# Kernel optimization log

Hardware: AMD Instinct MI355X
Metric: run time of the kernel (lower is better)

Reference implementation:

```python
import jax, jax.numpy as jnp
import numpy as np

INPUT_SIZE = 24
HIDDEN = 128
N_LAYERS = 2
OUT_SIZE = 1


def setup_inputs() -> dict:
    key = jax.random.key(0)
    ks = jax.random.split(key, 2 + 4 * N_LAYERS + 2)
    x = jax.random.normal(ks[0], (2048, 128, INPUT_SIZE), dtype=jnp.float32)
    params = {}
    s = 1.0 / np.sqrt(HIDDEN)
    idx = 1
    for l in range(N_LAYERS):
        in_dim = INPUT_SIZE if l == 0 else HIDDEN
        params[f"W_ih{l}"] = jax.random.uniform(ks[idx], (4 * HIDDEN, in_dim), minval=-s, maxval=s, dtype=jnp.float32); idx += 1
        params[f"W_hh{l}"] = jax.random.uniform(ks[idx], (4 * HIDDEN, HIDDEN), minval=-s, maxval=s, dtype=jnp.float32); idx += 1
        params[f"b_ih{l}"] = jax.random.uniform(ks[idx], (4 * HIDDEN,), minval=-s, maxval=s, dtype=jnp.float32); idx += 1
        params[f"b_hh{l}"] = jax.random.uniform(ks[idx], (4 * HIDDEN,), minval=-s, maxval=s, dtype=jnp.float32); idx += 1
    params["W_fc"] = jax.random.uniform(ks[idx], (OUT_SIZE, HIDDEN), minval=-s, maxval=s, dtype=jnp.float32); idx += 1
    params["b_fc"] = jax.random.uniform(ks[idx], (OUT_SIZE,), minval=-s, maxval=s, dtype=jnp.float32)
    return {"x": x, **params}


def _lstm_layer(x, W_ih, W_hh, b_ih, b_hh):
    # x: [B, T, in] -> outputs [B, T, H]. PyTorch gate order: i, f, g, o.
    B = x.shape[0]
    H = W_hh.shape[1]
    # precompute input projections for all timesteps: [T, B, 4H]
    xproj = jnp.einsum('bti,gi->tbg', x, W_ih) + b_ih + b_hh

    def step(carry, xp_t):
        h, c = carry
        gates = xp_t + h @ W_hh.T  # [B, 4H]
        i, f, g, o = jnp.split(gates, 4, axis=-1)
        i = jax.nn.sigmoid(i)
        f = jax.nn.sigmoid(f)
        g = jnp.tanh(g)
        o = jax.nn.sigmoid(o)
        c = f * c + i * g
        h = o * jnp.tanh(c)
        return (h, c), h

    h0 = jnp.zeros((B, H), dtype=x.dtype)
    c0 = jnp.zeros((B, H), dtype=x.dtype)
    (_, _), hs = jax.lax.scan(step, (h0, c0), xproj)
    return jnp.transpose(hs, (1, 0, 2))  # [B, T, H]


def reference(x, W_ih0, W_hh0, b_ih0, b_hh0, W_ih1, W_hh1, b_ih1, b_hh1, W_fc, b_fc):
    # Inference-mode forward: inter-layer dropout (p=0.2) is identity in eval.
    h1 = _lstm_layer(x, W_ih0, W_hh0, b_ih0, b_hh0)   # [B, T, H]
    h2 = _lstm_layer(h1, W_ih1, W_hh1, b_ih1, b_hh1)  # [B, T, H]
    last = h2[:, -1, :]                               # [B, H]
    return last @ W_fc.T + b_fc                       # [B, 1]
```

## Files before the change

kernel.cpp:

```cpp
#include <hip/hip_runtime.h>

#define TSTEPS 128
#define NIN 24
#define HD 128
#define BT 16
#define NBLK 128
#define NTH 512

#define RS    136
#define SLOT  (BT*RS)
#define H1B   (2*SLOT)
#define W1B   (4*SLOT)
#define SM_ELTS (W1B + 8*16*512)
#define SM_BYTES (SM_ELTS*2)

typedef _Float16 half8  __attribute__((ext_vector_type(8)));
typedef _Float16 half4v __attribute__((ext_vector_type(4)));
typedef float    floatx4 __attribute__((ext_vector_type(4)));

__device__ __forceinline__ float sigf(float x) {
    return __builtin_amdgcn_rcpf(1.0f + __expf(-x));
}
__device__ __forceinline__ float tanh_f(float x) {
    return 1.0f - 2.0f * __builtin_amdgcn_rcpf(1.0f + __expf(2.0f * x));
}

__device__ __forceinline__ half8 ldw8(const float* p) {
    const float4* q = (const float4*)p;
    float4 a = q[0], b = q[1];
    half8 r;
    r[0] = (_Float16)a.x; r[1] = (_Float16)a.y; r[2] = (_Float16)a.z; r[3] = (_Float16)a.w;
    r[4] = (_Float16)b.x; r[5] = (_Float16)b.y; r[6] = (_Float16)b.z; r[7] = (_Float16)b.w;
    return r;
}

__global__ __launch_bounds__(NTH, 2)
void lstm2_fused(const float* __restrict__ x,
                 const float* __restrict__ Wih0, const float* __restrict__ Whh0,
                 const float* __restrict__ bih0, const float* __restrict__ bhh0,
                 const float* __restrict__ Wih1, const float* __restrict__ Whh1,
                 const float* __restrict__ bih1, const float* __restrict__ bhh1,
                 const float* __restrict__ Wfc,  const float* __restrict__ bfc,
                 float* __restrict__ out)
{
    extern __shared__ __align__(16) _Float16 SM[];

    const int tid = threadIdx.x;
    const int blk = blockIdx.x;
    const int wv  = tid >> 6;
    const int ln  = tid & 63;
    const int qd  = ln >> 4;
    const int nn  = ln & 15;
    const int b0  = blk * BT;
    const int jc  = wv * 16 + nn;

    const half8 z8 = {0, 0, 0, 0, 0, 0, 0, 0};

    for (int i = tid * 8; i < W1B; i += NTH * 8) *(half8*)&SM[i] = z8;

    float bias0[4], bias1[4];
    half8 wih0[4];
    half8 whh0[4][4];
    half8 wih1[4][4];
#pragma unroll
    for (int tI = 0; tI < 4; ++tI) {
        int g = tI * HD + wv * 16 + nn;
        bias0[tI] = bih0[g] + bhh0[g];
        bias1[tI] = bih1[g] + bhh1[g];
        wih0[tI] = (qd < 3) ? ldw8(Wih0 + g * NIN + qd * 8) : z8;
#pragma unroll
        for (int kk = 0; kk < 4; ++kk) {
            whh0[tI][kk] = ldw8(Whh0 + g * HD + kk * 32 + qd * 8);
            wih1[tI][kk] = ldw8(Wih1 + g * HD + kk * 32 + qd * 8);
        }
    }

    for (int i = tid; i < 512 * 32; i += NTH) {
        int g  = i >> 5;
        int k0 = (i & 31) << 2;
        float4 v = *(const float4*)(Whh1 + g * HD + k0);
        half4v h; h[0] = (_Float16)v.x; h[1] = (_Float16)v.y;
                  h[2] = (_Float16)v.z; h[3] = (_Float16)v.w;
        int dst = W1B + ((((g >> 4) & 7) * 16) + (g >> 7) * 4 + (k0 >> 5)) * 512
                      + (((k0 >> 3) & 3) * 16 + (g & 15)) * 8 + (k0 & 7);
        *(half4v*)&SM[dst] = h;
    }

    const float* xrow = x + (size_t)(b0 + nn) * (TSTEPS * NIN) + (qd < 3 ? qd * 8 : 16);
    float4 pf0 = *(const float4*)(xrow);
    float4 pf1 = *(const float4*)(xrow + 4);

    float cs0[4] = {0.f, 0.f, 0.f, 0.f};
    float cs1[4] = {0.f, 0.f, 0.f, 0.f};
    const int w1base = W1B + wv * 8192 + ln * 8;

    __syncthreads();

    {
        half8 ax;
        ax[0] = (_Float16)pf0.x; ax[1] = (_Float16)pf0.y; ax[2] = (_Float16)pf0.z; ax[3] = (_Float16)pf0.w;
        ax[4] = (_Float16)pf1.x; ax[5] = (_Float16)pf1.y; ax[6] = (_Float16)pf1.z; ax[7] = (_Float16)pf1.w;
        pf0 = *(const float4*)(xrow + NIN);
        pf1 = *(const float4*)(xrow + NIN + 4);

        floatx4 acc0[4];
#pragma unroll
        for (int tI = 0; tI < 4; ++tI) {
            floatx4 a0 = {bias0[tI], bias0[tI], bias0[tI], bias0[tI]};
            acc0[tI] = __builtin_amdgcn_mfma_f32_16x16x32_f16(ax, wih0[tI], a0, 0, 0, 0);
        }
#pragma unroll
        for (int r = 0; r < 4; ++r) {
            float iv = sigf(acc0[0][r]);
            float gv = tanh_f(acc0[2][r]);
            float ov = sigf(acc0[3][r]);
            float cn = iv * gv;
            cs0[r] = cn;
            SM[(qd * 4 + r) * RS + jc] = (_Float16)(ov * tanh_f(cn));
        }
    }

#pragma unroll 1
    for (int t = 1; t < TSTEPS; ++t) {
        __syncthreads();

        half8 ax;
        ax[0] = (_Float16)pf0.x; ax[1] = (_Float16)pf0.y; ax[2] = (_Float16)pf0.z; ax[3] = (_Float16)pf0.w;
        ax[4] = (_Float16)pf1.x; ax[5] = (_Float16)pf1.y; ax[6] = (_Float16)pf1.z; ax[7] = (_Float16)pf1.w;
        {
            const int tn = (t < TSTEPS - 1) ? t + 1 : TSTEPS - 1;
            pf0 = *(const float4*)(xrow + tn * NIN);
            pf1 = *(const float4*)(xrow + tn * NIN + 4);
        }

        const int h0r = ((t - 1) & 1) * SLOT;
        const int h0w = (t & 1) * SLOT;
        const int h1r = H1B + (t & 1) * SLOT;
        const int h1w = H1B + ((t & 1) ^ 1) * SLOT;

        floatx4 acc0[4], acc1[4];
#pragma unroll
        for (int tI = 0; tI < 4; ++tI) {
            floatx4 a0 = {bias0[tI], bias0[tI], bias0[tI], bias0[tI]};
            acc0[tI] = __builtin_amdgcn_mfma_f32_16x16x32_f16(ax, wih0[tI], a0, 0, 0, 0);
            floatx4 a1 = {bias1[tI], bias1[tI], bias1[tI], bias1[tI]};
            acc1[tI] = a1;
        }

#pragma unroll
        for (int kk = 0; kk < 4; ++kk) {
            const half8 ah = *(const half8*)&SM[h0r + nn * RS + kk * 32 + qd * 8];
#pragma unroll
            for (int tI = 0; tI < 4; ++tI)
                acc0[tI] = __builtin_amdgcn_mfma_f32_16x16x32_f16(ah, whh0[tI][kk], acc0[tI], 0, 0, 0);
#pragma unroll
            for (int tI = 0; tI < 4; ++tI)
                acc1[tI] = __builtin_amdgcn_mfma_f32_16x16x32_f16(ah, wih1[tI][kk], acc1[tI], 0, 0, 0);
        }

#pragma unroll
        for (int kk = 0; kk < 4; ++kk) {
            const half8 a2 = *(const half8*)&SM[h1r + nn * RS + kk * 32 + qd * 8];
#pragma unroll
            for (int tI = 0; tI < 4; ++tI) {
                const half8 w1 = *(const half8*)&SM[w1base + (tI * 4 + kk) * 512];
                acc1[tI] = __builtin_amdgcn_mfma_f32_16x16x32_f16(a2, w1, acc1[tI], 0, 0, 0);
            }
        }

#pragma unroll
        for (int r = 0; r < 4; ++r) {
            float iv = sigf(acc0[0][r]);
            float fv = sigf(acc0[1][r]);
            float gv = tanh_f(acc0[2][r]);
            float ov = sigf(acc0[3][r]);
            float cn = fv * cs0[r] + iv * gv;
            cs0[r] = cn;
            SM[h0w + (qd * 4 + r) * RS + jc] = (_Float16)(ov * tanh_f(cn));
        }
#pragma unroll
        for (int r = 0; r < 4; ++r) {
            float iv = sigf(acc1[0][r]);
            float fv = sigf(acc1[1][r]);
            float gv = tanh_f(acc1[2][r]);
            float ov = sigf(acc1[3][r]);
            float cn = fv * cs1[r] + iv * gv;
            cs1[r] = cn;
            SM[h1w + (qd * 4 + r) * RS + jc] = (_Float16)(ov * tanh_f(cn));
        }
    }

    {
        __syncthreads();
        floatx4 acc1[4];
#pragma unroll
        for (int tI = 0; tI < 4; ++tI) {
            floatx4 a1 = {bias1[tI], bias1[tI], bias1[tI], bias1[tI]};
            acc1[tI] = a1;
        }
#pragma unroll
        for (int kk = 0; kk < 4; ++kk) {
            const half8 ah = *(const half8*)&SM[SLOT + nn * RS + kk * 32 + qd * 8];
#pragma unroll
            for (int tI = 0; tI < 4; ++tI)
                acc1[tI] = __builtin_amdgcn_mfma_f32_16x16x32_f16(ah, wih1[tI][kk], acc1[tI], 0, 0, 0);
        }
#pragma unroll
        for (int kk = 0; kk < 4; ++kk) {
            const half8 a2 = *(const half8*)&SM[H1B + nn * RS + kk * 32 + qd * 8];
#pragma unroll
            for (int tI = 0; tI < 4; ++tI) {
                const half8 w1 = *(const half8*)&SM[w1base + (tI * 4 + kk) * 512];
                acc1[tI] = __builtin_amdgcn_mfma_f32_16x16x32_f16(a2, w1, acc1[tI], 0, 0, 0);
            }
        }
#pragma unroll
        for (int r = 0; r < 4; ++r) {
            float iv = sigf(acc1[0][r]);
            float fv = sigf(acc1[1][r]);
            float gv = tanh_f(acc1[2][r]);
            float ov = sigf(acc1[3][r]);
            float cn = fv * cs1[r] + iv * gv;
            SM[H1B + SLOT + (qd * 4 + r) * RS + jc] = (_Float16)(ov * tanh_f(cn));
        }
    }
    __syncthreads();

    {
        int b = tid >> 5, sub = tid & 31;
        const _Float16* hp = &SM[H1B + SLOT + b * RS + sub * 4];
        const float4 wv4 = *(const float4*)(Wfc + sub * 4);
        float s = (float)hp[0] * wv4.x + (float)hp[1] * wv4.y
                + (float)hp[2] * wv4.z + (float)hp[3] * wv4.w;
        s += __shfl_down(s, 16, 32);
        s += __shfl_down(s, 8, 32);
        s += __shfl_down(s, 4, 32);
        s += __shfl_down(s, 2, 32);
        s += __shfl_down(s, 1, 32);
        if (sub == 0) out[b0 + b] = s + bfc[0];
    }
}

extern "C" void kernel_launch(void* const* d_in, const int* in_sizes, int n_in,
                              void* d_out, int out_size, void* d_ws, size_t ws_size,
                              hipStream_t stream) {
    static bool attr_set = false;
    if (!attr_set) {
        hipFuncSetAttribute(reinterpret_cast<const void*>(&lstm2_fused),
                            hipFuncAttributeMaxDynamicSharedMemorySize, SM_BYTES);
        attr_set = true;
    }
    const float* x    = (const float*)d_in[0];
    const float* Wih0 = (const float*)d_in[1];
    const float* Whh0 = (const float*)d_in[2];
    const float* bih0 = (const float*)d_in[3];
    const float* bhh0 = (const float*)d_in[4];
    const float* Wih1 = (const float*)d_in[5];
    const float* Whh1 = (const float*)d_in[6];
    const float* bih1 = (const float*)d_in[7];
    const float* bhh1 = (const float*)d_in[8];
    const float* Wfc  = (const float*)d_in[9];
    const float* bfc  = (const float*)d_in[10];
    float* out = (float*)d_out;

    lstm2_fused<<<dim3(NBLK), dim3(NTH), SM_BYTES, stream>>>(
        x, Wih0, Whh0, bih0, bhh0, Wih1, Whh1, bih1, bhh1, Wfc, bfc, out);
}
```

Before: 365.9 us.

## Keep Whh1 in registers and swap MFMA operands for vectorized h stores

Loads the layer-1 recurrent weights into per-thread registers instead of staging them in LDS, removing 16 LDS weight reads per step and shrinking shared memory to a static buffer. It swaps the MFMA A/B operands so each lane owns four consecutive hidden units, which allows a single 8-byte h store and per-row bias vectors. It also raises wave priority around the MFMA block. The cost is much higher VGPR pressure (four 4x4 half8 weight arrays per thread), which could cause spills given launch_bounds(512,2).

```diff
diff --git a/kernel.cpp b/kernel.cpp
--- a/kernel.cpp
+++ b/kernel.cpp
@@ -10,9 +10,7 @@
 #define RS    136
 #define SLOT  (BT*RS)
 #define H1B   (2*SLOT)
-#define W1B   (4*SLOT)
-#define SM_ELTS (W1B + 8*16*512)
-#define SM_BYTES (SM_ELTS*2)
+#define SM_ELTS (4*SLOT)
 
 typedef _Float16 half8  __attribute__((ext_vector_type(8)));
 typedef _Float16 half4v __attribute__((ext_vector_type(4)));
@@ -43,7 +41,7 @@
                  const float* __restrict__ Wfc,  const float* __restrict__ bfc,
                  float* __restrict__ out)
 {
-    extern __shared__ __align__(16) _Float16 SM[];
+    __shared__ __align__(16) _Float16 SM[SM_ELTS];
 
     const int tid = threadIdx.x;
     const int blk = blockIdx.x;
@@ -52,38 +50,35 @@
     const int qd  = ln >> 4;
     const int nn  = ln & 15;
     const int b0  = blk * BT;
-    const int jc  = wv * 16 + nn;
+    const int hcol = wv * 16 + qd * 4;
 
     const half8 z8 = {0, 0, 0, 0, 0, 0, 0, 0};
 
-    for (int i = tid * 8; i < W1B; i += NTH * 8) *(half8*)&SM[i] = z8;
-
-    float bias0[4], bias1[4];
+    for (int i = tid * 8; i < SM_ELTS; i += NTH * 8) *(half8*)&SM[i] = z8;
+
+    floatx4 bias0[4], bias1[4];
+#pragma unroll
+    for (int tI = 0; tI < 4; ++tI) {
+#pragma unroll
+        for (int r = 0; r < 4; ++r) {
+            int g = tI * HD + hcol + r;
+            bias0[tI][r] = bih0[g] + bhh0[g];
+            bias1[tI][r] = bih1[g] + bhh1[g];
+        }
+    }
+
     half8 wih0[4];
-    half8 whh0[4][4];
-    half8 wih1[4][4];
+    half8 whh0[4][4], wih1[4][4], whh1[4][4];
 #pragma unroll
     for (int tI = 0; tI < 4; ++tI) {
         int g = tI * HD + wv * 16 + nn;
-        bias0[tI] = bih0[g] + bhh0[g];
-        bias1[tI] = bih1[g] + bhh1[g];
         wih0[tI] = (qd < 3) ? ldw8(Wih0 + g * NIN + qd * 8) : z8;
 #pragma unroll
         for (int kk = 0; kk < 4; ++kk) {
             whh0[tI][kk] = ldw8(Whh0 + g * HD + kk * 32 + qd * 8);
             wih1[tI][kk] = ldw8(Wih1 + g * HD + kk * 32 + qd * 8);
-        }
-    }
-
-    for (int i = tid; i < 512 * 32; i += NTH) {
-        int g  = i >> 5;
-        int k0 = (i & 31) << 2;
-        float4 v = *(const float4*)(Whh1 + g * HD + k0);
-        half4v h; h[0] = (_Float16)v.x; h[1] = (_Float16)v.y;
-                  h[2] = (_Float16)v.z; h[3] = (_Float16)v.w;
-        int dst = W1B + ((((g >> 4) & 7) * 16) + (g >> 7) * 4 + (k0 >> 5)) * 512
-                      + (((k0 >> 3) & 3) * 16 + (g & 15)) * 8 + (k0 & 7);
-        *(half4v*)&SM[dst] = h;
+            whh1[tI][kk] = ldw8(Whh1 + g * HD + kk * 32 + qd * 8);
+        }
     }
 
     const float* xrow = x + (size_t)(b0 + nn) * (TSTEPS * NIN) + (qd < 3 ? qd * 8 : 16);
@@ -92,7 +87,6 @@
 
     float cs0[4] = {0.f, 0.f, 0.f, 0.f};
     float cs1[4] = {0.f, 0.f, 0.f, 0.f};
-    const int w1base = W1B + wv * 8192 + ln * 8;
 
     __syncthreads();
 
@@ -105,10 +99,10 @@
 
         floatx4 acc0[4];
 #pragma unroll
-        for (int tI = 0; tI < 4; ++tI) {
-            floatx4 a0 = {bias0[tI], bias0[tI], bias0[tI], bias0[tI]};
-            acc0[tI] = __builtin_amdgcn_mfma_f32_16x16x32_f16(ax, wih0[tI], a0, 0, 0, 0);
-        }
+        for (int tI = 0; tI < 4; ++tI)
+            acc0[tI] = __builtin_amdgcn_mfma_f32_16x16x32_f16(wih0[tI], ax, bias0[tI], 0, 0, 0);
+
+        half4v hw;
 #pragma unroll
         for (int r = 0; r < 4; ++r) {
             float iv = sigf(acc0[0][r]);
@@ -116,8 +110,9 @@
             float ov = sigf(acc0[3][r]);
             float cn = iv * gv;
             cs0[r] = cn;
-            SM[(qd * 4 + r) * RS + jc] = (_Float16)(ov * tanh_f(cn));
-        }
+            hw[r] = (_Float16)(ov * tanh_f(cn));
+        }
+        *(half4v*)&SM[0 * SLOT + nn * RS + hcol] = hw;
     }
 
 #pragma unroll 1
@@ -141,43 +136,82 @@
         floatx4 acc0[4], acc1[4];
 #pragma unroll
         for (int tI = 0; tI < 4; ++tI) {
-            floatx4 a0 = {bias0[tI], bias0[tI], bias0[tI], bias0[tI]};
-            acc0[tI] = __builtin_amdgcn_mfma_f32_16x16x32_f16(ax, wih0[tI], a0, 0, 0, 0);
-            floatx4 a1 = {bias1[tI], bias1[tI], bias1[tI], bias1[tI]};
-            acc1[tI] = a1;
-        }
-
+            acc0[tI] = __builtin_amdgcn_mfma_f32_16x16x32_f16(wih0[tI], ax, bias0[tI], 0, 0, 0);
+            acc1[tI] = bias1[tI];
+        }
+
+        __builtin_amdgcn_s_setprio(1);
 #pragma unroll
         for (int kk = 0; kk < 4; ++kk) {
             const half8 ah = *(const half8*)&SM[h0r + nn * RS + kk * 32 + qd * 8];
 #pragma unroll
             for (int tI = 0; tI < 4; ++tI)
-                acc0[tI] = __builtin_amdgcn_mfma_f32_16x16x32_f16(ah, whh0[tI][kk], acc0[tI], 0, 0, 0);
-#pragma unroll
-            for (int tI = 0; tI < 4; ++tI)
-                acc1[tI] = __builtin_amdgcn_mfma_f32_16x16x32_f16(ah, wih1[tI][kk], acc1[tI], 0, 0, 0);
-        }
-
+                acc0[tI] = __builtin_amdgcn_mfma_f32_16x16x32_f16(whh0[tI][kk], ah, acc0[tI], 0, 0, 0);
+#pragma unroll
+            for (int tI = 0; tI < 4; ++tI)
+                acc1[tI] = __builtin_amdgcn_mfma_f32_16x16x32_f16(wih1[tI][kk], ah, acc1[tI], 0, 0, 0);
+        }
 #pragma unroll
         for (int kk = 0; kk < 4; ++kk) {
             const half8 a2 = *(const half8*)&SM[h1r + nn * RS + kk * 32 + qd * 8];
 #pragma unroll
-            for (int tI = 0; tI < 4; ++tI) {
-                const half8 w1 = *(const half8*)&SM[w1base + (tI * 4 + kk) * 512];
-                acc1[tI] = __builtin_amdgcn_mfma_f32_16x16x32_f16(a2, w1, acc1[tI], 0, 0, 0);
+            for (int tI = 0; tI < 4; ++tI)
+                acc1[tI] = __builtin_amdgcn_mfma_f32_16x16x32_f16(whh1[tI][kk], a2, acc1[tI], 0, 0, 0);
+        }
+        __builtin_amdgcn_s_setprio(0);
+
+        {
+            half4v hw;
+#pragma unroll
+            for (int r = 0; r < 4; ++r) {
+                float iv = sigf(acc0[0][r]);
+                float fv = sigf(acc0[1][r]);
+                float gv = tanh_f(acc0[2][r]);
+                float ov = sigf(acc0[3][r]);
+                float cn = fv * cs0[r] + iv * gv;
+                cs0[r] = cn;
+                hw[r] = (_Float16)(ov * tanh_f(cn));
             }
-        }
-
-#pragma unroll
-        for (int r = 0; r < 4; ++r) {
-            float iv = sigf(acc0[0][r]);
-            float fv = sigf(acc0[1][r]);
-            float gv = tanh_f(acc0[2][r]);
-            float ov = sigf(acc0[3][r]);
-            float cn = fv * cs0[r] + iv * gv;
-            cs0[r] = cn;
-            SM[h0w + (qd * 4 + r) * RS + jc] = (_Float16)(ov * tanh_f(cn));
-        }
+            *(half4v*)&SM[h0w + nn * RS + hcol] = hw;
+        }
+        {
+            half4v hw;
+#pragma unroll
+            for (int r = 0; r < 4; ++r) {
+                float iv = sigf(acc1[0][r]);
+                float fv = sigf(acc1[1][r]);
+                float gv = tanh_f(acc1[2][r]);
+                float ov = sigf(acc1[3][r]);
+                float cn = fv * cs1[r] + iv * gv;
+                cs1[r] = cn;
+                hw[r] = (_Float16)(ov * tanh_f(cn));
+            }
+            *(half4v*)&SM[h1w + nn * RS + hcol] = hw;
+        }
+    }
+
+    {
+        __syncthreads();
+        floatx4 acc1[4];
+#pragma unroll
+        for (int tI = 0; tI < 4; ++tI) acc1[tI] = bias1[tI];
+
+#pragma unroll
+        for (int kk = 0; kk < 4; ++kk) {
+            const half8 ah = *(const half8*)&SM[SLOT + nn * RS + kk * 32 + qd * 8];
+#pragma unroll
+            for (int tI = 0; tI < 4; ++tI)
+                acc1[tI] = __builtin_amdgcn_mfma_f32_16x16x32_f16(wih1[tI][kk], ah, acc1[tI], 0, 0, 0);
+        }
+#pragma unroll
+        for (int kk = 0; kk < 4; ++kk) {
+            const half8 a2 = *(const half8*)&SM[H1B + nn * RS + kk * 32 + qd * 8];
+#pragma unroll
+            for (int tI = 0; tI < 4; ++tI)
+                acc1[tI] = __builtin_amdgcn_mfma_f32_16x16x32_f16(whh1[tI][kk], a2, acc1[tI], 0, 0, 0);
+        }
+
+        half4v hw;
 #pragma unroll
         for (int r = 0; r < 4; ++r) {
             float iv = sigf(acc1[0][r]);
@@ -185,44 +219,9 @@
             float gv = tanh_f(acc1[2][r]);
             float ov = sigf(acc1[3][r]);
             float cn = fv * cs1[r] + iv * gv;
-            cs1[r] = cn;
-            SM[h1w + (qd * 4 + r) * RS + jc] = (_Float16)(ov * tanh_f(cn));
-        }
-    }
-
-    {
-        __syncthreads();
-        floatx4 acc1[4];
-#pragma unroll
-        for (int tI = 0; tI < 4; ++tI) {
-            floatx4 a1 = {bias1[tI], bias1[tI], bias1[tI], bias1[tI]};
-            acc1[tI] = a1;
-        }
-#pragma unroll
-        for (int kk = 0; kk < 4; ++kk) {
-            const half8 ah = *(const half8*)&SM[SLOT + nn * RS + kk * 32 + qd * 8];
-#pragma unroll
-            for (int tI = 0; tI < 4; ++tI)
-                acc1[tI] = __builtin_amdgcn_mfma_f32_16x16x32_f16(ah, wih1[tI][kk], acc1[tI], 0, 0, 0);
-        }
-#pragma unroll
-        for (int kk = 0; kk < 4; ++kk) {
-            const half8 a2 = *(const half8*)&SM[H1B + nn * RS + kk * 32 + qd * 8];
-#pragma unroll
-            for (int tI = 0; tI < 4; ++tI) {
-                const half8 w1 = *(const half8*)&SM[w1base + (tI * 4 + kk) * 512];
-                acc1[tI] = __builtin_amdgcn_mfma_f32_16x16x32_f16(a2, w1, acc1[tI], 0, 0, 0);
-            }
-        }
-#pragma unroll
-        for (int r = 0; r < 4; ++r) {
-            float iv = sigf(acc1[0][r]);
-            float fv = sigf(acc1[1][r]);
-            float gv = tanh_f(acc1[2][r]);
-            float ov = sigf(acc1[3][r]);
-            float cn = fv * cs1[r] + iv * gv;
-            SM[H1B + SLOT + (qd * 4 + r) * RS + jc] = (_Float16)(ov * tanh_f(cn));
-        }
+            hw[r] = (_Float16)(ov * tanh_f(cn));
+        }
+        *(half4v*)&SM[H1B + SLOT + nn * RS + hcol] = hw;
     }
     __syncthreads();
 
@@ -244,12 +243,6 @@
 extern "C" void kernel_launch(void* const* d_in, const int* in_sizes, int n_in,
                               void* d_out, int out_size, void* d_ws, size_t ws_size,
                               hipStream_t stream) {
-    static bool attr_set = false;
-    if (!attr_set) {
-        hipFuncSetAttribute(reinterpret_cast<const void*>(&lstm2_fused),
-                            hipFuncAttributeMaxDynamicSharedMemorySize, SM_BYTES);
-        attr_set = true;
-    }
     const float* x    = (const float*)d_in[0];
     const float* Wih0 = (const float*)d_in[1];
     const float* Whh0 = (const float*)d_in[2];
@@ -263,6 +256,6 @@
     const float* bfc  = (const float*)d_in[10];
     float* out = (float*)d_out;
 
-    lstm2_fused<<<dim3(NBLK), dim3(NTH), SM_BYTES, stream>>>(
+    lstm2_fused<<<dim3(NBLK), dim3(NTH), 0, stream>>>(
         x, Wih0, Whh0, bih0, bhh0, Wih1, Whh1, bih1, bhh1, Wfc, bfc, out);
 }
```

Result: slower. 733.7 us (+100.5%).
